# Kernel optimization log

Hardware: AMD Instinct MI355X
Metric: run time of the kernel (lower is better)

The kernel has to match this reference:

```python
import jax, jax.numpy as jnp
import numpy as np

B, S, V = 16, 256, 32000
E, H, L, FFN, NC = 256, 8, 2, 1024, 4
DK = E // H
NQ = E  # n_qubits == hidden_dim == embed_dim (required by the module's shape constraints)
EPS = 1e-5


def qproj(x, theta):
    # Analytic simulation of: RX(x_k) encode + trainable RX(theta_k) + CNOT ladder + MeasureAll(PauliZ).
    # RX gates on the same wire compose; CNOT ladder maps Z_j -> Z_0...Z_j in Heisenberg picture, so
    # <Z_j> = prod_{k<=j} cos(x_k + theta_k)  (product state expectation).
    return jnp.cumprod(jnp.cos(x + theta), axis=-1)


def layernorm(x, g, b):
    m = x.mean(-1, keepdims=True)
    v = x.var(-1, keepdims=True)
    return (x - m) * jax.lax.rsqrt(v + EPS) * g + b


def sinusoidal_pe(seq, d):
    pos = jnp.arange(seq, dtype=jnp.float32)[:, None]
    div = jnp.exp(jnp.arange(0, d, 2, dtype=jnp.float32) * (-np.log(10000.0) / d))
    pe = jnp.zeros((seq, d), jnp.float32)
    pe = pe.at[:, 0::2].set(jnp.sin(pos * div)).at[:, 1::2].set(jnp.cos(pos * div))
    return pe


def _forward(x, token_emb, lstm_W, lstm_b, lstm_theta, ln1_g, ln1_b, ln2_g, ln2_b,
             qkv_theta, combine_W, combine_b, ffn_theta, lin1_W, lin1_b, lin2_W, lin2_b,
             cls_W, cls_b):
    emb = token_emb[x]  # (B, S, E)

    # --- QLSTM: each gate = linear -> quantum circuit -> nonlinearity ---
    def step(carry, xt):
        hx, cx = carry
        comb = jnp.concatenate([xt, hx], axis=-1)                      # (B, 2E)
        z = jnp.einsum('bd,gdq->gbq', comb, lstm_W) + lstm_b[:, None]  # (4, B, NQ)
        q = jnp.cumprod(jnp.cos(z + lstm_theta[:, None, :]), axis=-1)
        f = jax.nn.sigmoid(q[0])
        i = jax.nn.sigmoid(q[1])
        g = jnp.tanh(q[2])
        o = jax.nn.sigmoid(q[3])
        cx = f * cx + i * g
        hx = o * jnp.tanh(cx)
        return (hx, cx), hx

    h0 = jnp.zeros((emb.shape[0], NQ), emb.dtype)
    _, hs = jax.lax.scan(step, (h0, h0), jnp.swapaxes(emb, 0, 1))
    h = jnp.swapaxes(hs, 0, 1)  # (B, S, NQ)

    h = h + sinusoidal_pe(h.shape[1], E)[None]

    # --- quantum transformer blocks ---
    def heads(t):
        return t.reshape(t.shape[0], t.shape[1], H, DK).transpose(0, 2, 1, 3)

    for l in range(L):
        q = qproj(h, qkv_theta[l, 0])
        k = qproj(h, qkv_theta[l, 1])
        v = qproj(h, qkv_theta[l, 2])
        qh, kh, vh = heads(q), heads(k), heads(v)
        scores = jnp.einsum('bhqd,bhkd->bhqk', qh, kh) / jnp.sqrt(jnp.float32(DK))
        attn = jax.nn.softmax(scores, axis=-1)
        out = jnp.einsum('bhqk,bhkd->bhqd', attn, vh).transpose(0, 2, 1, 3).reshape(h.shape)
        out = out @ combine_W[l] + combine_b[l]
        h = layernorm(h + out, ln1_g[l], ln1_b[l])
        ff = qproj(h, ffn_theta[l]) @ lin1_W[l] + lin1_b[l]
        ff = jax.nn.relu(ff) @ lin2_W[l] + lin2_b[l]
        h = layernorm(h + ff, ln2_g[l], ln2_b[l])

    pooled = h.mean(axis=1)  # (B, E)
    return pooled @ cls_W + cls_b  # (B, NC)


def setup_inputs() -> dict:
    key = jax.random.key(0)
    ks = jax.random.split(key, 10)
    s = 0.05
    return {
        'x': jax.random.randint(ks[0], (B, S), 0, V),
        'token_emb': jax.random.normal(ks[1], (V, E), jnp.float32) * s,
        'lstm_W': jax.random.normal(ks[2], (4, 2 * E, NQ), jnp.float32) * s,
        'lstm_b': jnp.zeros((4, NQ), jnp.float32),
        'lstm_theta': jax.random.normal(ks[3], (4, NQ), jnp.float32) * s,
        'ln1_g': jnp.ones((L, E), jnp.float32),
        'ln1_b': jnp.zeros((L, E), jnp.float32),
        'ln2_g': jnp.ones((L, E), jnp.float32),
        'ln2_b': jnp.zeros((L, E), jnp.float32),
        'qkv_theta': jax.random.normal(ks[4], (L, 3, E), jnp.float32) * s,
        'combine_W': jax.random.normal(ks[5], (L, E, E), jnp.float32) * s,
        'combine_b': jnp.zeros((L, E), jnp.float32),
        'ffn_theta': jax.random.normal(ks[6], (L, E), jnp.float32) * s,
        'lin1_W': jax.random.normal(ks[7], (L, E, FFN), jnp.float32) * s,
        'lin1_b': jnp.zeros((L, FFN), jnp.float32),
        'lin2_W': jax.random.normal(ks[8], (L, FFN, E), jnp.float32) * s,
        'lin2_b': jnp.zeros((L, E), jnp.float32),
        'cls_W': jax.random.normal(ks[9], (E, NC), jnp.float32) * s,
        'cls_b': jnp.zeros((NC,), jnp.float32),
    }


def reference(x, token_emb, lstm_W, lstm_b, lstm_theta, ln1_g, ln1_b, ln2_g, ln2_b,
              qkv_theta, combine_W, combine_b, ffn_theta, lin1_W, lin1_b, lin2_W, lin2_b,
              cls_W, cls_b):
    return _forward(x, token_emb, lstm_W, lstm_b, lstm_theta, ln1_g, ln1_b, ln2_g, ln2_b,
                    qkv_theta, combine_W, combine_b, ffn_theta, lin1_W, lin1_b, lin2_W, lin2_b,
                    cls_W, cls_b)
```

## Files before the change

kernel.cpp:

```cpp
#include <hip/hip_runtime.h>
#include <hip/hip_bf16.h>


typedef __attribute__((ext_vector_type(8))) short bf8v;
typedef __attribute__((ext_vector_type(4))) float f4v;
#define MFMA16 __builtin_amdgcn_mfma_f32_16x16x32_bf16

__device__ __forceinline__ unsigned short f2bf(float f) {
  unsigned u = __builtin_bit_cast(unsigned, f);
  u += 0x7fffu + ((u >> 16) & 1u);
  return (unsigned short)(u >> 16);
}
__device__ __forceinline__ float rcp_f(float x) { return __builtin_amdgcn_rcpf(x); }
__device__ __forceinline__ float sigm(float x) { return rcp_f(1.f + __expf(-x)); }
__device__ __forceinline__ float tanh_f(float x) { return 1.f - 2.f * rcp_f(__expf(2.f * x) + 1.f); }

#define DOT2BF(acc, a, b) \
  asm("v_dot2_f32_bf16 %0, %1, %2, %0" : "+v"(acc) : "v"(a), "v"(b))

__global__ void embed_kernel(const int* __restrict__ x, const float* __restrict__ tab,
                             unsigned short* __restrict__ eb) {
  int tok = blockIdx.x, tid = threadIdx.x;
  eb[tok * 256 + tid] = f2bf(tab[x[tok] * 256 + tid]);
}

__global__ void pack_bt(const float* __restrict__ W, int K, int N,
                        unsigned short* __restrict__ Th, long wz, long tz) {
  __shared__ float tile[64][65];
  W += (long)blockIdx.z * wz;
  Th += (long)blockIdx.z * tz;
  int n0 = blockIdx.x * 64, k0 = blockIdx.y * 64;
  int tid = threadIdx.x, tx = tid & 63, ty = tid >> 6;
  for (int r = ty; r < 64; r += 4) tile[r][tx] = W[(k0 + r) * N + n0 + tx];
  __syncthreads();
  for (int r = ty; r < 64; r += 4) {
    Th[(n0 + r) * K + k0 + tx] = f2bf(tile[tx][r]);
  }
}

__global__ void pack_wreg_kernel(const float* __restrict__ lstmW, unsigned* __restrict__ Wreg) {
  int o = blockIdx.x * 256 + threadIdx.x;
  int c = o & 3;
  int q = (o >> 2) & 255;
  int i4 = (o >> 10) & 15;
  int gs = o >> 14;
  int gi = gs >> 1, s = gs & 1;
  int i = i4 * 4 + c;
  int d = s * 128 + 2 * i;
  unsigned lo = f2bf(lstmW[(gi * 512 + 256 + d) * 256 + q]);
  unsigned hi = f2bf(lstmW[(gi * 512 + 256 + d + 1) * 256 + q]);
  Wreg[o] = lo | (hi << 16);
}

__global__ void pack_wl_kernel(const float* __restrict__ lstmW, unsigned* __restrict__ WLg) {
  int o = blockIdx.x * 256 + threadIdx.x;
  int c = o & 3;
  int q = (o >> 2) & 255;
  int p4 = o >> 10;
  int d = 2 * (p4 * 4 + c);
  unsigned lo = f2bf(lstmW[(3 * 512 + 256 + d) * 256 + q]);
  unsigned hi = f2bf(lstmW[(3 * 512 + 256 + d + 1) * 256 + q]);
  WLg[o] = lo | (hi << 16);
}

__global__ void __launch_bounds__(256) gemm_mfma(const unsigned short* __restrict__ A,
                                                 const unsigned short* __restrict__ B,
                                                 const float* __restrict__ bias,
                                                 float* __restrict__ Cf,
                                                 unsigned short* __restrict__ Cb,
                                                 int M, int N, int K, int mode) {
  __shared__ unsigned short As[128 * 40];
  __shared__ unsigned short Bs[128 * 40];

  const int tid = threadIdx.x;
  const int lane = tid & 63;
  const int wid = tid >> 6;
  const int wr = wid >> 1, wc = wid & 1;
  const int bm = blockIdx.y * 128, bn = blockIdx.x * 128;

  const int srow = tid >> 2;
  const int scol = (tid & 3) * 8;

  f4v acc[4][4] = {};

  for (int kt = 0; kt < K; kt += 32) {
#pragma unroll
    for (int p = 0; p < 2; ++p) {
      int r = srow + p * 64;
      *(uint4*)(&As[r * 40 + scol]) = *(const uint4*)(&A[(bm + r) * K + kt + scol]);
      *(uint4*)(&Bs[r * 40 + scol]) = *(const uint4*)(&B[(bn + r) * K + kt + scol]);
    }
    __syncthreads();

    bf8v a[4], b[4];
    const int kq = (lane >> 4) * 8;
#pragma unroll
    for (int f = 0; f < 4; ++f) {
      a[f] = *(const bf8v*)(&As[(wr * 64 + f * 16 + (lane & 15)) * 40 + kq]);
      b[f] = *(const bf8v*)(&Bs[(wc * 64 + f * 16 + (lane & 15)) * 40 + kq]);
    }
#pragma unroll
    for (int fm = 0; fm < 4; ++fm)
#pragma unroll
      for (int fn = 0; fn < 4; ++fn)
        acc[fm][fn] = MFMA16(a[fm], b[fn], acc[fm][fn], 0, 0, 0);
    __syncthreads();
  }

#pragma unroll
  for (int fm = 0; fm < 4; ++fm)
#pragma unroll
    for (int fn = 0; fn < 4; ++fn) {
      int c = bn + wc * 64 + fn * 16 + (lane & 15);
      int r0 = bm + wr * 64 + fm * 16 + ((lane >> 4) << 2);
      float bv = bias[c];
#pragma unroll
      for (int j = 0; j < 4; ++j) {
        float v = acc[fm][fn][j] + bv;
        if (mode == 1) {
          Cb[(r0 + j) * N + c] = f2bf(fmaxf(v, 0.f));
        } else {
          Cf[(r0 + j) * N + c] = v;
        }
      }
    }
}

__global__ void
__attribute__((amdgpu_flat_work_group_size(512, 512), amdgpu_waves_per_eu(2, 2)))
lstm_kernel(const unsigned* __restrict__ Wreg,
            const unsigned* __restrict__ WLg,
            const float* __restrict__ lstmTh,
            const float* __restrict__ xw,
            float* __restrict__ hb) {
  extern __shared__ char smem[];
  unsigned* WL = (unsigned*)smem;
  float* part = (float*)(smem + 131072);
  float* qv = part + 2048;
  float* wtot = qv + 1024;
  unsigned* hp = (unsigned*)(wtot + 16);

  const int t = threadIdx.x;
  const int b = blockIdx.x;
  const int q = t & 255;
  const int s = t >> 8;
  const int lane = t & 63;
  const int w = t >> 6;

  {
    const uint4* src = (const uint4*)WLg;
    uint4* dst = (uint4*)WL;
    for (int j = t; j < 8192; j += 512) dst[j] = src[j];
  }
  const uint4* Wreg4 = (const uint4*)Wreg;
  uint4 wreg[48];
#pragma unroll
  for (int j = 0; j < 48; ++j) {
    int gi = j >> 4, i4 = j & 15;
    wreg[j] = Wreg4[((gi * 2 + s) * 16 + i4) * 256 + q];
  }
#pragma unroll
  for (int j = 0; j < 48; ++j) {
    asm volatile("" : "+v"(wreg[j].x), "+v"(wreg[j].y), "+v"(wreg[j].z), "+v"(wreg[j].w));
  }
  const float thA = lstmTh[t];
  const float thB = lstmTh[512 + t];
  float cx = 0.f;
  if (t < 128) hp[t] = 0u;
  __syncthreads();

  const int xbase = (b << 8) * 1024;
  const uint4* WL4 = (const uint4*)WL;
  const uint4* hp4 = (const uint4*)hp;

  float xa = xw[xbase + t];
  float xb = xw[xbase + 512 + t];

  for (int st = 0; st < 256; ++st) {
    int nx = (st < 255) ? st + 1 : 255;
    float xa_n = xw[xbase + nx * 1024 + t];
    float xb_n = xw[xbase + nx * 1024 + 512 + t];

    float a0 = 0.f, a1 = 0.f, a2 = 0.f, a3 = 0.f;
#pragma unroll
    for (int i4 = 0; i4 < 16; ++i4) {
      uint4 hh = hp4[(s << 4) + i4];
      uint4 w3 = WL4[((s << 4) + i4) * 256 + q];
      uint4 w0 = wreg[i4];
      uint4 w1 = wreg[16 + i4];
      uint4 w2 = wreg[32 + i4];
      DOT2BF(a0, w0.x, hh.x); DOT2BF(a0, w0.y, hh.y);
      DOT2BF(a0, w0.z, hh.z); DOT2BF(a0, w0.w, hh.w);
      DOT2BF(a1, w1.x, hh.x); DOT2BF(a1, w1.y, hh.y);
      DOT2BF(a1, w1.z, hh.z); DOT2BF(a1, w1.w, hh.w);
      DOT2BF(a2, w2.x, hh.x); DOT2BF(a2, w2.y, hh.y);
      DOT2BF(a2, w2.z, hh.z); DOT2BF(a2, w2.w, hh.w);
      DOT2BF(a3, w3.x, hh.x); DOT2BF(a3, w3.y, hh.y);
      DOT2BF(a3, w3.z, hh.z); DOT2BF(a3, w3.w, hh.w);
    }
    part[(0 * 2 + s) * 256 + q] = a0;
    part[(1 * 2 + s) * 256 + q] = a1;
    part[(2 * 2 + s) * 256 + q] = a2;
    part[(3 * 2 + s) * 256 + q] = a3;
    __syncthreads();

    int gA = s, gB = s + 2;
    float zA = part[(gA * 2 + 0) * 256 + q] + part[(gA * 2 + 1) * 256 + q] + xa + thA;
    float zB = part[(gB * 2 + 0) * 256 + q] + part[(gB * 2 + 1) * 256 + q] + xb + thB;
    float vA = __cosf(zA);
    float vB = __cosf(zB);
#pragma unroll
    for (int off = 1; off < 64; off <<= 1) {
      float oA = __shfl_up(vA, off, 64);
      float oB = __shfl_up(vB, off, 64);
      if (lane >= off) { vA *= oA; vB *= oB; }
    }
    if (lane == 63) { wtot[w * 2] = vA; wtot[w * 2 + 1] = vB; }
    qv[s * 256 + q] = vA;
    qv[512 + s * 256 + q] = vB;
    __syncthreads();

    if (t < 256) {
      int j = q >> 6;
      float p0 = 1.f, p1 = 1.f, p2 = 1.f, p3 = 1.f;
      for (int k = 0; k < j; ++k) {
        p0 *= wtot[2 * k];
        p1 *= wtot[2 * (4 + k)];
        p2 *= wtot[2 * k + 1];
        p3 *= wtot[2 * (4 + k) + 1];
      }
      float fg = sigm(qv[t] * p0);
      float ig = sigm(qv[256 + t] * p1);
      float gg = tanh_f(qv[512 + t] * p2);
      float og = sigm(qv[768 + t] * p3);
      cx = fg * cx + ig * gg;
      float hv = og * tanh_f(cx);
      hb[((b << 8) + st) * 256 + t] = hv;
      float nb = __shfl_xor(hv, 1, 64);
      if ((t & 1) == 0) hp[t >> 1] = (unsigned)f2bf(hv) | ((unsigned)f2bf(nb) << 16);
    }
    __syncthreads();
    xa = xa_n;
    xb = xb_n;
  }
}

__global__ void pe_add_kernel(float* __restrict__ h) {
  int tok = blockIdx.x, tid = threadIdx.x;
  int s = tok & 255;
  int j = tid >> 1;
  float div = __expf((float)j * -0.07195578415622253f);
  float ang = (float)s * div;
  float pe = (tid & 1) ? __cosf(ang) : __sinf(ang);
  h[tok * 256 + tid] += pe;
}

__global__ void qproj3_kernel(const float* __restrict__ hin, const float* __restrict__ thetas,
                              float* __restrict__ outbase) {
  __shared__ float wtot[4];
  int tok = blockIdx.x, y = blockIdx.y;
  int tid = threadIdx.x, lane = tid & 63, wid = tid >> 6;
  const float* theta = thetas + y * 256;
  float* out = outbase + (long)y * 1048576;
  float v = __cosf(hin[tok * 256 + tid] + theta[tid]);
#pragma unroll
  for (int off = 1; off < 64; off <<= 1) {
    float o = __shfl_up(v, off, 64);
    if (lane >= off) v *= o;
  }
  if (lane == 63) wtot[wid] = v;
  __syncthreads();
  float pre = 1.f;
  for (int w = 0; w < wid; ++w) pre *= wtot[w];
  out[tok * 256 + tid] = v * pre;
}

__global__ void qproj_bf_kernel(const float* __restrict__ hin, const float* __restrict__ theta,
                                unsigned short* __restrict__ outb) {
  __shared__ float wtot[4];
  int tok = blockIdx.x, tid = threadIdx.x, lane = tid & 63, wid = tid >> 6;
  float v = __cosf(hin[tok * 256 + tid] + theta[tid]);
#pragma unroll
  for (int off = 1; off < 64; off <<= 1) {
    float o = __shfl_up(v, off, 64);
    if (lane >= off) v *= o;
  }
  if (lane == 63) wtot[wid] = v;
  __syncthreads();
  float pre = 1.f;
  for (int w = 0; w < wid; ++w) pre *= wtot[w];
  outb[tok * 256 + tid] = f2bf(v * pre);
}

__global__ void __launch_bounds__(256, 1) attn_kernel(const float* __restrict__ qb,
                                                      const float* __restrict__ kb,
                                                      const float* __restrict__ vb,
                                                      unsigned short* __restrict__ outb) {
  extern __shared__ float sm[];
  float* Qs = sm;
  float* Ks = Qs + 256 * 36;
  float* Vs = Ks + 256 * 36;
  float* ps = Vs + 32 * 260;
  int hd = blockIdx.x, b = blockIdx.y;
  int tid = threadIdx.x, lane = tid & 63, wid = tid >> 6;
  const float scale = 0.17677669529663687f;

  for (int i = tid; i < 256 * 32; i += 256) {
    int r = i >> 5, d = i & 31;
    int src = (b * 256 + r) * 256 + hd * 32 + d;
    Qs[r * 36 + d] = qb[src];
    Ks[r * 36 + d] = kb[src];
    Vs[d * 260 + r] = vb[src];
  }
  __syncthreads();

  float* pw = ps + wid * 256;
  for (int r = wid; r < 256; r += 4) {
    float4 qreg[8];
    const float4* qrow = (const float4*)(Qs + r * 36);
#pragma unroll
    for (int i = 0; i < 8; ++i) qreg[i] = qrow[i];
    float s[4];
#pragma unroll
    for (int j = 0; j < 4; ++j) {
      int k = lane + 64 * j;
      const float4* kr = (const float4*)(Ks + k * 36);
      float a = 0.f;
#pragma unroll
      for (int i = 0; i < 8; ++i) {
        float4 kv = kr[i];
        a += qreg[i].x * kv.x + qreg[i].y * kv.y + qreg[i].z * kv.z + qreg[i].w * kv.w;
      }
      s[j] = a * scale;
    }
    float m = fmaxf(fmaxf(s[0], s[1]), fmaxf(s[2], s[3]));
#pragma unroll
    for (int off = 32; off; off >>= 1) m = fmaxf(m, __shfl_xor(m, off, 64));
    float p[4], sum = 0.f;
#pragma unroll
    for (int j = 0; j < 4; ++j) { p[j] = __expf(s[j] - m); sum += p[j]; }
#pragma unroll
    for (int off = 32; off; off >>= 1) sum += __shfl_xor(sum, off, 64);
    float inv = rcp_f(sum);
#pragma unroll
    for (int j = 0; j < 4; ++j) pw[lane + 64 * j] = p[j] * inv;
    int d = lane & 31, half = lane >> 5;
    const float4* pv = (const float4*)(pw + half * 128);
    const float4* v4 = (const float4*)(Vs + d * 260 + half * 128);
    float a = 0.f;
#pragma unroll
    for (int i = 0; i < 32; ++i) {
      float4 pp = pv[i];
      float4 vv = v4[i];
      a += pp.x * vv.x + pp.y * vv.y + pp.z * vv.z + pp.w * vv.w;
    }
    a += __shfl_down(a, 32, 64);
    if (lane < 32) outb[(b * 256 + r) * 256 + hd * 32 + d] = f2bf(a);
  }
}

__global__ void ln_kernel(float* __restrict__ hio, const float* __restrict__ delta,
                          const float* __restrict__ gamma, const float* __restrict__ beta) {
  __shared__ float red[16];
  int tok = blockIdx.x, tid = threadIdx.x, lane = tid & 63, wid = tid >> 6;
  float v = hio[tok * 256 + tid] + delta[tok * 256 + tid];
  float s1 = v, s2 = v * v;
#pragma unroll
  for (int off = 32; off; off >>= 1) {
    s1 += __shfl_xor(s1, off, 64);
    s2 += __shfl_xor(s2, off, 64);
  }
  if (lane == 0) { red[wid] = s1; red[wid + 8] = s2; }
  __syncthreads();
  float t1 = red[0] + red[1] + red[2] + red[3];
  float t2 = red[8] + red[9] + red[10] + red[11];
  float mean = t1 * (1.f / 256.f);
  float var = t2 * (1.f / 256.f) - mean * mean;
  float w = rsqrtf(var + 1e-5f);
  hio[tok * 256 + tid] = (v - mean) * w * gamma[tid] + beta[tid];
}

__global__ void pool_cls_kernel(const float* __restrict__ h, const float* __restrict__ clsW,
                                const float* __restrict__ clsb, float* __restrict__ out) {
  __shared__ float pl[256];
  __shared__ float red[8];
  int b = blockIdx.x, tid = threadIdx.x, lane = tid & 63, wid = tid >> 6;
  float s = 0.f;
  for (int t = 0; t < 256; ++t) s += h[(b * 256 + t) * 256 + tid];
  pl[tid] = s * (1.f / 256.f);
  __syncthreads();
  for (int c = 0; c < 4; ++c) {
    float v = pl[tid] * clsW[tid * 4 + c];
#pragma unroll
    for (int off = 32; off; off >>= 1) v += __shfl_xor(v, off, 64);
    if (lane == 0) red[wid] = v;
    __syncthreads();
    if (tid == 0) out[b * 4 + c] = red[0] + red[1] + red[2] + red[3] + clsb[c];
    __syncthreads();
  }
}

extern "C" void kernel_launch(void* const* d_in, const int* in_sizes, int n_in,
                              void* d_out, int out_size, void* d_ws, size_t ws_size,
                              hipStream_t stream) {
  const int* x = (const int*)d_in[0];
  const float* token_emb = (const float*)d_in[1];
  const float* lstm_W = (const float*)d_in[2];
  const float* lstm_b = (const float*)d_in[3];
  const float* lstm_th = (const float*)d_in[4];
  const float* ln1_g = (const float*)d_in[5];
  const float* ln1_b = (const float*)d_in[6];
  const float* ln2_g = (const float*)d_in[7];
  const float* ln2_b = (const float*)d_in[8];
  const float* qkv_th = (const float*)d_in[9];
  const float* comb_W = (const float*)d_in[10];
  const float* comb_b = (const float*)d_in[11];
  const float* ffn_th = (const float*)d_in[12];
  const float* lin1_W = (const float*)d_in[13];
  const float* lin1_b = (const float*)d_in[14];
  const float* lin2_W = (const float*)d_in[15];
  const float* lin2_b = (const float*)d_in[16];
  const float* cls_W = (const float*)d_in[17];
  const float* cls_b = (const float*)d_in[18];

  float* ws = (float*)d_ws;
  typedef unsigned short ushort_t;
  ushort_t* emb_b = (ushort_t*)ws;
  ushort_t* att_b = emb_b;
  float* xw = ws + 1048576;
  ushort_t* ffh_b = (ushort_t*)xw;
  float* hb = ws + 5242880;
  float* qq = ws + 6291456;
  float* kk = ws + 7340032;
  float* vv = ws + 8388608;
  float* tmp = ws + 9437184;
  unsigned* Wreg = (unsigned*)tmp;
  unsigned* WLg = (unsigned*)(tmp + 98304);
  ushort_t* ffq_b = (ushort_t*)(ws + 10485760);
  ushort_t* wxt_b = (ushort_t*)(ws + 11534336);
  ushort_t* cmb_b = wxt_b + 262144;
  ushort_t* l1_b = cmb_b + 131072;
  ushort_t* l2_b = l1_b + 524288;

  const int LSTM_LDS = 131072 + 8192 + 4096 + 64 + 512;
  const int ATT_LDS = (256 * 36 * 2 + 32 * 260 + 4 * 256) * 4;
  (void)hipFuncSetAttribute(reinterpret_cast<const void*>(lstm_kernel),
                            hipFuncAttributeMaxDynamicSharedMemorySize, LSTM_LDS);
  (void)hipFuncSetAttribute(reinterpret_cast<const void*>(attn_kernel),
                            hipFuncAttributeMaxDynamicSharedMemorySize, ATT_LDS);

  embed_kernel<<<4096, 256, 0, stream>>>(x, token_emb, emb_b);
  pack_wreg_kernel<<<384, 256, 0, stream>>>(lstm_W, Wreg);
  pack_wl_kernel<<<128, 256, 0, stream>>>(lstm_W, WLg);
  pack_bt<<<dim3(4, 4, 4), 256, 0, stream>>>(lstm_W, 256, 256, wxt_b, 131072, 65536);
  pack_bt<<<dim3(4, 4, 2), 256, 0, stream>>>(comb_W, 256, 256, cmb_b, 65536, 65536);
  pack_bt<<<dim3(16, 4, 2), 256, 0, stream>>>(lin1_W, 256, 1024, l1_b, 262144, 262144);
  pack_bt<<<dim3(4, 16, 2), 256, 0, stream>>>(lin2_W, 1024, 256, l2_b, 262144, 262144);

  gemm_mfma<<<dim3(8, 32), 256, 0, stream>>>(emb_b, wxt_b, lstm_b,
                                             xw, nullptr, 4096, 1024, 256, 0);
  lstm_kernel<<<16, 512, LSTM_LDS, stream>>>(Wreg, WLg, lstm_th, xw, hb);
  pe_add_kernel<<<4096, 256, 0, stream>>>(hb);

  for (int l = 0; l < 2; ++l) {
    qproj3_kernel<<<dim3(4096, 3), 256, 0, stream>>>(hb, qkv_th + l * 768, qq);
    attn_kernel<<<dim3(8, 16), 256, ATT_LDS, stream>>>(qq, kk, vv, att_b);
    gemm_mfma<<<dim3(2, 32), 256, 0, stream>>>(att_b, cmb_b + l * 65536, comb_b + l * 256,
                                               tmp, nullptr, 4096, 256, 256, 0);
    ln_kernel<<<4096, 256, 0, stream>>>(hb, tmp, ln1_g + l * 256, ln1_b + l * 256);
    qproj_bf_kernel<<<4096, 256, 0, stream>>>(hb, ffn_th + l * 256, ffq_b);
    gemm_mfma<<<dim3(8, 32), 256, 0, stream>>>(ffq_b, l1_b + l * 262144, lin1_b + l * 1024,
                                               nullptr, ffh_b, 4096, 1024, 256, 1);
    gemm_mfma<<<dim3(2, 32), 256, 0, stream>>>(ffh_b, l2_b + l * 262144, lin2_b + l * 256,
                                               tmp, nullptr, 4096, 256, 1024, 0);
    ln_kernel<<<4096, 256, 0, stream>>>(hb, tmp, ln2_g + l * 256, ln2_b + l * 256);
  }

  pool_cls_kernel<<<16, 256, 0, stream>>>(hb, cls_W, cls_b, (float*)d_out);
}
```

Baseline: 1.273 ms.

## Split LSTM gates across four blocks with global-memory exchange; fuse LN with qproj

The recurrent LSTM kernel previously ran one 512-thread block per batch element, holding three gate weight sets in registers and one in LDS. It now launches four blocks per batch element, one per gate, each keeping only its own gate's weights in LDS. The blocks exchange gate activations every timestep through tagged 64-bit atomic stores and spin-loads in global memory. This spreads the serial recurrence over more CUs at the cost of a cross-block handshake per step, and it relies on all 64 blocks being resident at once to avoid deadlock. Separately, layernorm and the FFN quantum projection are fused into one kernel, removing a launch and a round trip through global memory.

```diff
diff --git a/kernel.cpp b/kernel.cpp
--- a/kernel.cpp
+++ b/kernel.cpp
@@ -38,29 +38,16 @@
   }
 }
 
-__global__ void pack_wreg_kernel(const float* __restrict__ lstmW, unsigned* __restrict__ Wreg) {
-  int o = blockIdx.x * 256 + threadIdx.x;
-  int c = o & 3;
-  int q = (o >> 2) & 255;
-  int i4 = (o >> 10) & 15;
-  int gs = o >> 14;
-  int gi = gs >> 1, s = gs & 1;
-  int i = i4 * 4 + c;
-  int d = s * 128 + 2 * i;
-  unsigned lo = f2bf(lstmW[(gi * 512 + 256 + d) * 256 + q]);
-  unsigned hi = f2bf(lstmW[(gi * 512 + 256 + d + 1) * 256 + q]);
-  Wreg[o] = lo | (hi << 16);
-}
-
 __global__ void pack_wl_kernel(const float* __restrict__ lstmW, unsigned* __restrict__ WLg) {
+  int gate = blockIdx.y;
   int o = blockIdx.x * 256 + threadIdx.x;
   int c = o & 3;
   int q = (o >> 2) & 255;
   int p4 = o >> 10;
   int d = 2 * (p4 * 4 + c);
-  unsigned lo = f2bf(lstmW[(3 * 512 + 256 + d) * 256 + q]);
-  unsigned hi = f2bf(lstmW[(3 * 512 + 256 + d + 1) * 256 + q]);
-  WLg[o] = lo | (hi << 16);
+  unsigned lo = f2bf(lstmW[(gate * 512 + 256 + d) * 256 + q]);
+  unsigned hi = f2bf(lstmW[(gate * 512 + 256 + d + 1) * 256 + q]);
+  WLg[gate * 32768 + o] = lo | (hi << 16);
 }
 
 __global__ void __launch_bounds__(256) gemm_mfma(const unsigned short* __restrict__ A,
@@ -126,122 +113,112 @@
     }
 }
 
-__global__ void
-__attribute__((amdgpu_flat_work_group_size(512, 512), amdgpu_waves_per_eu(2, 2)))
-lstm_kernel(const unsigned* __restrict__ Wreg,
-            const unsigned* __restrict__ WLg,
+__global__ void __launch_bounds__(512)
+lstm_kernel(const unsigned* __restrict__ WLgAll,
             const float* __restrict__ lstmTh,
             const float* __restrict__ xw,
-            float* __restrict__ hb) {
+            float* __restrict__ hb,
+            unsigned long long* __restrict__ qex) {
   extern __shared__ char smem[];
   unsigned* WL = (unsigned*)smem;
   float* part = (float*)(smem + 131072);
-  float* qv = part + 2048;
-  float* wtot = qv + 1024;
-  unsigned* hp = (unsigned*)(wtot + 16);
+  float* wtot = part + 512;
+  unsigned* hp = (unsigned*)(wtot + 8);
 
   const int t = threadIdx.x;
-  const int b = blockIdx.x;
+  const int b = blockIdx.x >> 2;
+  const int g = blockIdx.x & 3;
   const int q = t & 255;
   const int s = t >> 8;
   const int lane = t & 63;
   const int w = t >> 6;
 
   {
-    const uint4* src = (const uint4*)WLg;
+    const uint4* src = (const uint4*)WLgAll + g * 8192;
     uint4* dst = (uint4*)WL;
     for (int j = t; j < 8192; j += 512) dst[j] = src[j];
   }
-  const uint4* Wreg4 = (const uint4*)Wreg;
-  uint4 wreg[48];
-#pragma unroll
-  for (int j = 0; j < 48; ++j) {
-    int gi = j >> 4, i4 = j & 15;
-    wreg[j] = Wreg4[((gi * 2 + s) * 16 + i4) * 256 + q];
-  }
-#pragma unroll
-  for (int j = 0; j < 48; ++j) {
-    asm volatile("" : "+v"(wreg[j].x), "+v"(wreg[j].y), "+v"(wreg[j].z), "+v"(wreg[j].w));
-  }
-  const float thA = lstmTh[t];
-  const float thB = lstmTh[512 + t];
+  const float th = lstmTh[g * 256 + q];
   float cx = 0.f;
   if (t < 128) hp[t] = 0u;
   __syncthreads();
 
-  const int xbase = (b << 8) * 1024;
   const uint4* WL4 = (const uint4*)WL;
   const uint4* hp4 = (const uint4*)hp;
-
-  float xa = xw[xbase + t];
-  float xb = xw[xbase + 512 + t];
+  const int xrow = (b << 8) * 1024 + g * 256 + q;
 
   for (int st = 0; st < 256; ++st) {
-    int nx = (st < 255) ? st + 1 : 255;
-    float xa_n = xw[xbase + nx * 1024 + t];
-    float xb_n = xw[xbase + nx * 1024 + 512 + t];
-
-    float a0 = 0.f, a1 = 0.f, a2 = 0.f, a3 = 0.f;
+    float xv = xw[xrow + st * 1024];
+
+    float acc = 0.f;
 #pragma unroll
     for (int i4 = 0; i4 < 16; ++i4) {
       uint4 hh = hp4[(s << 4) + i4];
-      uint4 w3 = WL4[((s << 4) + i4) * 256 + q];
-      uint4 w0 = wreg[i4];
-      uint4 w1 = wreg[16 + i4];
-      uint4 w2 = wreg[32 + i4];
-      DOT2BF(a0, w0.x, hh.x); DOT2BF(a0, w0.y, hh.y);
-      DOT2BF(a0, w0.z, hh.z); DOT2BF(a0, w0.w, hh.w);
-      DOT2BF(a1, w1.x, hh.x); DOT2BF(a1, w1.y, hh.y);
-      DOT2BF(a1, w1.z, hh.z); DOT2BF(a1, w1.w, hh.w);
-      DOT2BF(a2, w2.x, hh.x); DOT2BF(a2, w2.y, hh.y);
-      DOT2BF(a2, w2.z, hh.z); DOT2BF(a2, w2.w, hh.w);
-      DOT2BF(a3, w3.x, hh.x); DOT2BF(a3, w3.y, hh.y);
-      DOT2BF(a3, w3.z, hh.z); DOT2BF(a3, w3.w, hh.w);
-    }
-    part[(0 * 2 + s) * 256 + q] = a0;
-    part[(1 * 2 + s) * 256 + q] = a1;
-    part[(2 * 2 + s) * 256 + q] = a2;
-    part[(3 * 2 + s) * 256 + q] = a3;
-    __syncthreads();
-
-    int gA = s, gB = s + 2;
-    float zA = part[(gA * 2 + 0) * 256 + q] + part[(gA * 2 + 1) * 256 + q] + xa + thA;
-    float zB = part[(gB * 2 + 0) * 256 + q] + part[(gB * 2 + 1) * 256 + q] + xb + thB;
-    float vA = __cosf(zA);
-    float vB = __cosf(zB);
-#pragma unroll
-    for (int off = 1; off < 64; off <<= 1) {
-      float oA = __shfl_up(vA, off, 64);
-      float oB = __shfl_up(vB, off, 64);
-      if (lane >= off) { vA *= oA; vB *= oB; }
-    }
-    if (lane == 63) { wtot[w * 2] = vA; wtot[w * 2 + 1] = vB; }
-    qv[s * 256 + q] = vA;
-    qv[512 + s * 256 + q] = vB;
-    __syncthreads();
-
+      uint4 wv = WL4[((s << 4) + i4) * 256 + q];
+      DOT2BF(acc, wv.x, hh.x); DOT2BF(acc, wv.y, hh.y);
+      DOT2BF(acc, wv.z, hh.z); DOT2BF(acc, wv.w, hh.w);
+    }
+    part[s * 256 + q] = acc;
+    __syncthreads();
+
+    float v = 0.f;
     if (t < 256) {
-      int j = q >> 6;
-      float p0 = 1.f, p1 = 1.f, p2 = 1.f, p3 = 1.f;
-      for (int k = 0; k < j; ++k) {
-        p0 *= wtot[2 * k];
-        p1 *= wtot[2 * (4 + k)];
-        p2 *= wtot[2 * k + 1];
-        p3 *= wtot[2 * (4 + k) + 1];
+      float z = part[q] + part[256 + q] + xv + th;
+      v = __cosf(z);
+#pragma unroll
+      for (int off = 1; off < 64; off <<= 1) {
+        float o = __shfl_up(v, off, 64);
+        if (lane >= off) v *= o;
       }
-      float fg = sigm(qv[t] * p0);
-      float ig = sigm(qv[256 + t] * p1);
-      float gg = tanh_f(qv[512 + t] * p2);
-      float og = sigm(qv[768 + t] * p3);
-      cx = fg * cx + ig * gg;
+      if (lane == 63) wtot[w] = v;
+    }
+    __syncthreads();
+
+    if (t < 256) {
+      {
+        float p = 1.f;
+        int j = q >> 6;
+        for (int k = 0; k < j; ++k) p *= wtot[k];
+        v *= p;
+      }
+      const unsigned tag = (unsigned)(st + 1);
+      const int par = st & 1;
+      unsigned long long pk =
+          ((unsigned long long)__builtin_bit_cast(unsigned, v) << 32) | tag;
+      __hip_atomic_store(&qex[(((par * 16 + b) * 4 + g) << 8) + q], pk,
+                         __ATOMIC_RELAXED, __HIP_MEMORY_SCOPE_AGENT);
+      float q0v = 0.f, q1v = 0.f, q2v = 0.f, q3v = 0.f;
+#pragma unroll
+      for (int gg = 0; gg < 4; ++gg) {
+        float val;
+        if (gg == g) {
+          val = v;
+        } else {
+          unsigned long long got;
+          for (;;) {
+            got = __hip_atomic_load(&qex[(((par * 16 + b) * 4 + gg) << 8) + q],
+                                    __ATOMIC_RELAXED, __HIP_MEMORY_SCOPE_AGENT);
+            if ((unsigned)got == tag) break;
+            __builtin_amdgcn_s_sleep(1);
+          }
+          val = __builtin_bit_cast(float, (unsigned)(got >> 32));
+        }
+        if (gg == 0) q0v = val;
+        else if (gg == 1) q1v = val;
+        else if (gg == 2) q2v = val;
+        else q3v = val;
+      }
+      float fg = sigm(q0v);
+      float ig = sigm(q1v);
+      float gg_ = tanh_f(q2v);
+      float og = sigm(q3v);
+      cx = fg * cx + ig * gg_;
       float hv = og * tanh_f(cx);
-      hb[((b << 8) + st) * 256 + t] = hv;
+      if (g == 0) hb[((b << 8) + st) * 256 + q] = hv;
       float nb = __shfl_xor(hv, 1, 64);
       if ((t & 1) == 0) hp[t >> 1] = (unsigned)f2bf(hv) | ((unsigned)f2bf(nb) << 16);
     }
     __syncthreads();
-    xa = xa_n;
-    xb = xb_n;
   }
 }
 
@@ -275,21 +252,40 @@
   out[tok * 256 + tid] = v * pre;
 }
 
-__global__ void qproj_bf_kernel(const float* __restrict__ hin, const float* __restrict__ theta,
+__global__ void ln_qproj_kernel(float* __restrict__ hio, const float* __restrict__ delta,
+                                const float* __restrict__ gamma, const float* __restrict__ beta,
+                                const float* __restrict__ theta,
                                 unsigned short* __restrict__ outb) {
+  __shared__ float red[16];
   __shared__ float wtot[4];
   int tok = blockIdx.x, tid = threadIdx.x, lane = tid & 63, wid = tid >> 6;
-  float v = __cosf(hin[tok * 256 + tid] + theta[tid]);
+  float v = hio[tok * 256 + tid] + delta[tok * 256 + tid];
+  float s1 = v, s2 = v * v;
+#pragma unroll
+  for (int off = 32; off; off >>= 1) {
+    s1 += __shfl_xor(s1, off, 64);
+    s2 += __shfl_xor(s2, off, 64);
+  }
+  if (lane == 0) { red[wid] = s1; red[wid + 8] = s2; }
+  __syncthreads();
+  float t1 = red[0] + red[1] + red[2] + red[3];
+  float t2 = red[8] + red[9] + red[10] + red[11];
+  float mean = t1 * (1.f / 256.f);
+  float var = t2 * (1.f / 256.f) - mean * mean;
+  float w = rsqrtf(var + 1e-5f);
+  float val = (v - mean) * w * gamma[tid] + beta[tid];
+  hio[tok * 256 + tid] = val;
+  float c = __cosf(val + theta[tid]);
 #pragma unroll
   for (int off = 1; off < 64; off <<= 1) {
-    float o = __shfl_up(v, off, 64);
-    if (lane >= off) v *= o;
-  }
-  if (lane == 63) wtot[wid] = v;
+    float o = __shfl_up(c, off, 64);
+    if (lane >= off) c *= o;
+  }
+  if (lane == 63) wtot[wid] = c;
   __syncthreads();
   float pre = 1.f;
-  for (int w = 0; w < wid; ++w) pre *= wtot[w];
-  outb[tok * 256 + tid] = f2bf(v * pre);
+  for (int k = 0; k < wid; ++k) pre *= wtot[k];
+  outb[tok * 256 + tid] = f2bf(c * pre);
 }
 
 __global__ void __launch_bounds__(256, 1) attn_kernel(const float* __restrict__ qb,
@@ -434,24 +430,25 @@
   float* kk = ws + 7340032;
   float* vv = ws + 8388608;
   float* tmp = ws + 9437184;
-  unsigned* Wreg = (unsigned*)tmp;
-  unsigned* WLg = (unsigned*)(tmp + 98304);
+  unsigned* WLg = (unsigned*)tmp;
   ushort_t* ffq_b = (ushort_t*)(ws + 10485760);
   ushort_t* wxt_b = (ushort_t*)(ws + 11534336);
   ushort_t* cmb_b = wxt_b + 262144;
   ushort_t* l1_b = cmb_b + 131072;
   ushort_t* l2_b = l1_b + 524288;
-
-  const int LSTM_LDS = 131072 + 8192 + 4096 + 64 + 512;
+  unsigned long long* qex = (unsigned long long*)(ws + 12255232);
+
+  const int LSTM_LDS = 131072 + 2048 + 32 + 512;
   const int ATT_LDS = (256 * 36 * 2 + 32 * 260 + 4 * 256) * 4;
   (void)hipFuncSetAttribute(reinterpret_cast<const void*>(lstm_kernel),
                             hipFuncAttributeMaxDynamicSharedMemorySize, LSTM_LDS);
   (void)hipFuncSetAttribute(reinterpret_cast<const void*>(attn_kernel),
                             hipFuncAttributeMaxDynamicSharedMemorySize, ATT_LDS);
 
+  hipMemsetAsync(qex, 0, 2 * 16 * 4 * 256 * 8, stream);
+
   embed_kernel<<<4096, 256, 0, stream>>>(x, token_emb, emb_b);
-  pack_wreg_kernel<<<384, 256, 0, stream>>>(lstm_W, Wreg);
-  pack_wl_kernel<<<128, 256, 0, stream>>>(lstm_W, WLg);
+  pack_wl_kernel<<<dim3(128, 4), 256, 0, stream>>>(lstm_W, WLg);
   pack_bt<<<dim3(4, 4, 4), 256, 0, stream>>>(lstm_W, 256, 256, wxt_b, 131072, 65536);
   pack_bt<<<dim3(4, 4, 2), 256, 0, stream>>>(comb_W, 256, 256, cmb_b, 65536, 65536);
   pack_bt<<<dim3(16, 4, 2), 256, 0, stream>>>(lin1_W, 256, 1024, l1_b, 262144, 262144);
@@ -459,7 +456,7 @@
 
   gemm_mfma<<<dim3(8, 32), 256, 0, stream>>>(emb_b, wxt_b, lstm_b,
                                              xw, nullptr, 4096, 1024, 256, 0);
-  lstm_kernel<<<16, 512, LSTM_LDS, stream>>>(Wreg, WLg, lstm_th, xw, hb);
+  lstm_kernel<<<64, 512, LSTM_LDS, stream>>>(WLg, lstm_th, xw, hb, qex);
   pe_add_kernel<<<4096, 256, 0, stream>>>(hb);
 
   for (int l = 0; l < 2; ++l) {
@@ -467,8 +464,8 @@
     attn_kernel<<<dim3(8, 16), 256, ATT_LDS, stream>>>(qq, kk, vv, att_b);
     gemm_mfma<<<dim3(2, 32), 256, 0, stream>>>(att_b, cmb_b + l * 65536, comb_b + l * 256,
                                                tmp, nullptr, 4096, 256, 256, 0);
-    ln_kernel<<<4096, 256, 0, stream>>>(hb, tmp, ln1_g + l * 256, ln1_b + l * 256);
-    qproj_bf_kernel<<<4096, 256, 0, stream>>>(hb, ffn_th + l * 256, ffq_b);
+    ln_qproj_kernel<<<4096, 256, 0, stream>>>(hb, tmp, ln1_g + l * 256, ln1_b + l * 256,
+                                              ffn_th + l * 256, ffq_b);
     gemm_mfma<<<dim3(8, 32), 256, 0, stream>>>(ffq_b, l1_b + l * 262144, lin1_b + l * 1024,
                                                nullptr, ffh_b, 4096, 1024, 256, 1);
     gemm_mfma<<<dim3(2, 32), 256, 0, stream>>>(ffh_b, l2_b + l * 262144, lin2_b + l * 256,
```

New measurement: 1.192 ms. -6.4%, faster.
